# Kernel tuning notes

Hardware: AMD Instinct MI355X
Metric: run time of the kernel (lower is better)

## Reference

```python
import math
import jax, jax.numpy as jnp
import numpy as np

D_MODEL = 1024
NUM_SCALES = 4
STATE_SIZE = 16
EXPAND = 2
D_INNER = D_MODEL * EXPAND
D_PER_SCALE = D_INNER // NUM_SCALES
BATCH, SEQ = 4, 4096


def _make_A_log():
    base = np.arange(1, STATE_SIZE + 1, dtype=np.float32)  # (N,)
    parts = [np.broadcast_to(base * (2.0 ** i), (D_PER_SCALE, STATE_SIZE)) for i in range(NUM_SCALES)]
    A = np.concatenate(parts, axis=0)  # (d_inner, N)
    return jnp.asarray(np.log(A))


def setup_inputs() -> dict:
    key = jax.random.key(0)
    ks = jax.random.split(key, 8)
    scale = 0.02
    x = jax.random.normal(ks[0], (BATCH, SEQ, D_MODEL), dtype=jnp.float32)
    W_in = jax.random.normal(ks[1], (2 * D_INNER, D_MODEL), dtype=jnp.float32) * scale
    W_B = jax.random.normal(ks[2], (STATE_SIZE, D_INNER), dtype=jnp.float32) * scale
    W_C = jax.random.normal(ks[3], (STATE_SIZE, D_INNER), dtype=jnp.float32) * scale
    W_dt = jax.random.normal(ks[4], (D_INNER, D_INNER), dtype=jnp.float32) * scale
    # dt bias: log of dt_init ~ Uniform in log-space between 1e-3 and 1e-1
    u = jax.random.uniform(ks[5], (D_INNER,), dtype=jnp.float32)
    b_dt = u * (math.log(0.1) - math.log(0.001)) + math.log(0.001)
    W_out = jax.random.normal(ks[6], (D_MODEL, D_INNER), dtype=jnp.float32) * scale
    A_log = _make_A_log()
    D = jnp.ones((D_INNER,), dtype=jnp.float32)
    output_gate = jnp.zeros((1,), dtype=jnp.float32)
    return {"x": x, "W_in": W_in, "A_log": A_log, "W_B": W_B, "W_C": W_C,
            "W_dt": W_dt, "b_dt": b_dt, "D": D, "output_gate": output_gate, "W_out": W_out}


def _selective_scan(x_ssm, A, B_mat, C_mat, dt):
    # x_ssm: (B,L,d), A: (d,N), B_mat/C_mat: (B,L,N), dt: (B,L,d)
    b, L, d = x_ssm.shape
    N = A.shape[1]
    h0 = jnp.zeros((b, d, N), dtype=jnp.float32)

    def step(h, inp):
        dt_t, B_t, C_t, x_t = inp  # (B,d),(B,N),(B,N),(B,d)
        A_bar = jnp.exp(jnp.minimum(dt_t[..., None] * A, 20.0))       # (B,d,N)
        B_bar = dt_t[..., None] * B_t[:, None, :]                      # (B,d,N)
        h = A_bar * h + B_bar * x_t[..., None]
        y_t = jnp.einsum('bdn,bn->bd', h, C_t)
        return h, y_t

    xs = (jnp.swapaxes(dt, 0, 1), jnp.swapaxes(B_mat, 0, 1),
          jnp.swapaxes(C_mat, 0, 1), jnp.swapaxes(x_ssm, 0, 1))
    _, ys = jax.lax.scan(step, h0, xs)   # ys: (L,B,d)
    return jnp.swapaxes(ys, 0, 1)


def reference(x, W_in, A_log, W_B, W_C, W_dt, b_dt, D, output_gate, W_out):
    xz = jnp.einsum('bld,ed->ble', x, W_in)          # (B,L,2*d_inner)
    x_ssm, z = jnp.split(xz, 2, axis=-1)
    A = -jnp.exp(A_log.astype(jnp.float32))           # (d_inner,N)
    B_mat = jnp.einsum('bld,nd->bln', x_ssm, W_B)
    C_mat = jnp.einsum('bld,nd->bln', x_ssm, W_C)
    dt = jax.nn.softplus(jnp.einsum('bld,ed->ble', x_ssm, W_dt) + b_dt)
    y = _selective_scan(x_ssm.astype(jnp.float32), A,
                        B_mat.astype(jnp.float32), C_mat.astype(jnp.float32),
                        dt.astype(jnp.float32))
    y = y + x_ssm * D[None, None, :]
    y = y * jax.nn.silu(z)
    out = jnp.einsum('ble,de->bld', y, W_out) * jax.nn.sigmoid(output_gate)
    return out
```

## Files before the change

### kernel.cpp

```cpp
#include <hip/hip_runtime.h>
#include <hip/hip_bf16.h>
#include <math.h>

#define D_MODEL 1024
#define D_INNER 2048
#define NSTATE  16
#define BATCH   4
#define SEQ     4096
#define MTOT    (BATCH*SEQ)
#define SDT     2176
#define NCAT    2176
#define NCHUNK  16
#define CLEN    (SEQ/NCHUNK)
#define N1      (2*D_INNER)

typedef __attribute__((ext_vector_type(8))) __bf16 bf16x8;
typedef __attribute__((ext_vector_type(4))) float f32x4;

__device__ __forceinline__ float b2f(unsigned short u){
  return __uint_as_float(((unsigned int)u) << 16);
}
__device__ __forceinline__ unsigned short f2b(float f){
  unsigned int u = __float_as_uint(f);
  u = (u + 0x7FFFu + ((u >> 16) & 1u)) >> 16;
  return (unsigned short)u;
}
__device__ __forceinline__ float softplus_f(float x){
  float r = log1pf(__expf(-fabsf(x)));
  return x > 0.f ? x + r : r;
}

__device__ __forceinline__ void async16(unsigned short* lds, const unsigned short* g){
  __builtin_amdgcn_global_load_lds(
      (const __attribute__((address_space(1))) unsigned int*)g,
      (__attribute__((address_space(3))) unsigned int*)lds, 16, 0, 0);
}

__global__ void cvt_f2b_kernel(const float* __restrict__ src,
                               unsigned short* __restrict__ dst){
  int i = (blockIdx.x * 256 + threadIdx.x) * 4;
  float4 v = *(const float4*)(src + i);
  *(ushort2*)(dst + i)     = (ushort2){f2b(v.x), f2b(v.y)};
  *(ushort2*)(dst + i + 2) = (ushort2){f2b(v.z), f2b(v.w)};
}

__global__ void concat_w_kernel(const float* __restrict__ Wdt,
                                const float* __restrict__ WB,
                                const float* __restrict__ WC,
                                unsigned short* __restrict__ Wcat){
  int idx = blockIdx.x * 256 + threadIdx.x;
  int row = idx >> 9;
  int q   = idx & 511;
  float4 v;
  if      (row < 2048) v = *(const float4*)(Wdt + ((size_t)row * 2048 + q * 4));
  else if (row < 2064) v = *(const float4*)(WB  + ((size_t)(row - 2048) * 2048 + q * 4));
  else if (row < 2080) v = *(const float4*)(WC  + ((size_t)(row - 2064) * 2048 + q * 4));
  else                 v = make_float4(0.f, 0.f, 0.f, 0.f);
  unsigned short* p = Wcat + (size_t)idx * 4;
  *(ushort2*)(p)     = (ushort2){f2b(v.x), f2b(v.y)};
  *(ushort2*)(p + 2) = (ushort2){f2b(v.z), f2b(v.w)};
}

template<int MODE, int K>
__global__ __launch_bounds__(512, 1) void gemm_bt(
    const unsigned short* __restrict__ A,
    const unsigned short* __restrict__ W,
    unsigned short* __restrict__ o0,
    unsigned short* __restrict__ o1,
    float* __restrict__ of,
    const float* __restrict__ bias)
{
  const int tid  = threadIdx.x;
  const int lane = tid & 63;
  const int w    = tid >> 6;
  const int wm   = w >> 2;
  const int wn   = w & 3;
  const int m16  = lane & 15, q = lane >> 4;

  const int gx  = gridDim.x;
  const int nwg = gx * gridDim.y;
  int flat = blockIdx.y * gx + blockIdx.x;
  flat = (flat & 7) * (nwg >> 3) + (flat >> 3);
  const int bm = flat / gx;
  const int bn = flat - bm * gx;

  __shared__ unsigned short sA[2][16384];
  __shared__ unsigned short sB[2][8192];

  f32x4 acc[8][2];
  #pragma unroll
  for (int i = 0; i < 8; i++)
    #pragma unroll
    for (int j = 0; j < 2; j++) acc[i][j] = (f32x4){0.f, 0.f, 0.f, 0.f};

  const int ch = (tid & 7) ^ ((tid >> 3) & 7);
  const unsigned short* Ag = A + (size_t)(bm * 256 + (tid >> 3)) * K + ch * 8;
  const unsigned short* Wg = W + (size_t)(bn * 128 + (tid >> 3)) * K + ch * 8;

#define STAGE_A(buf, h, t) do { \
    async16(&sA[buf][(h)*8192 + w*512],        Ag + (size_t)((h)*128    )*K + (t)*64); \
    async16(&sA[buf][(h)*8192 + 4096 + w*512], Ag + (size_t)((h)*128 + 64)*K + (t)*64); \
  } while(0)
#define STAGE_B(buf, t) do { \
    async16(&sB[buf][w*512],        Wg + (size_t)(t)*64); \
    async16(&sB[buf][4096 + w*512], Wg + (size_t)64*K + (t)*64); \
  } while(0)

#define LDA(dst, buf, mh) do { \
    _Pragma("unroll") for (int mt = 0; mt < 4; mt++) \
    _Pragma("unroll") for (int kk = 0; kk < 2; kk++) { \
      const int row_ = wm*128 + (mh)*64 + mt*16 + m16; \
      dst[mt][kk] = *(const bf16x8*)&sA[buf][row_*64 + (((kk*4 + q) ^ (m16 & 7)) << 3)]; \
    } } while(0)
#define LDB(dst, buf) do { \
    _Pragma("unroll") for (int nt = 0; nt < 2; nt++) \
    _Pragma("unroll") for (int kk = 0; kk < 2; kk++) { \
      const int row_ = wn*32 + nt*16 + m16; \
      dst[nt][kk] = *(const bf16x8*)&sB[buf][row_*64 + (((kk*4 + q) ^ (m16 & 7)) << 3)]; \
    } } while(0)

#define MMAQ(Aa, Bb, MH) do { \
    __builtin_amdgcn_s_setprio(1); \
    _Pragma("unroll") for (int kk = 0; kk < 2; kk++) \
    _Pragma("unroll") for (int mt = 0; mt < 4; mt++) \
    _Pragma("unroll") for (int nt = 0; nt < 2; nt++) \
      acc[(MH)*4 + mt][nt] = __builtin_amdgcn_mfma_f32_16x16x32_bf16( \
          Aa[mt][kk], Bb[nt][kk], acc[(MH)*4 + mt][nt], 0, 0, 0); \
    __builtin_amdgcn_s_setprio(0); \
    __builtin_amdgcn_sched_barrier(0); \
  } while(0)

#define BAR()  asm volatile("s_barrier" ::: "memory")
#define LGK0() do { asm volatile("s_waitcnt lgkmcnt(0)" ::: "memory"); \
                    __builtin_amdgcn_sched_barrier(0); } while(0)

  STAGE_A(0, 0, 0); STAGE_A(0, 1, 0); STAGE_B(0, 0);
  STAGE_A(1, 0, 1); STAGE_A(1, 1, 1);
  asm volatile("s_waitcnt vmcnt(4)" ::: "memory");
  BAR();

  auto run_iter = [&](int t0, bool last) {
    bf16x8 a[4][2], b[2][2];
    LDA(a, 0, 0); LDB(b, 0);
    STAGE_B(1, t0 + 1);
    BAR(); LGK0();
    MMAQ(a, b, 0);
    BAR();
    LDA(a, 0, 1);
    if (!last) { STAGE_A(0, 0, t0 + 2); STAGE_A(0, 1, t0 + 2); }
    BAR(); LGK0();
    MMAQ(a, b, 1);
    if (last) asm volatile("s_waitcnt vmcnt(0)" ::: "memory");
    else      asm volatile("s_waitcnt vmcnt(4)" ::: "memory");
    BAR();
    LDA(a, 1, 0); LDB(b, 1);
    if (!last) STAGE_B(0, t0 + 2);
    BAR(); LGK0();
    MMAQ(a, b, 0);
    BAR();
    LDA(a, 1, 1);
    if (!last) { STAGE_A(1, 0, t0 + 3); STAGE_A(1, 1, t0 + 3); }
    BAR(); LGK0();
    MMAQ(a, b, 1);
    if (!last) asm volatile("s_waitcnt vmcnt(4)" ::: "memory");
    BAR();
  };

  const int NIT = K >> 7;
  #pragma unroll 1
  for (int j = 0; j < NIT - 1; j++) run_iter(2 * j, false);
  run_iter(2 * (NIT - 1), true);

  float gscale = 1.f;
  if (MODE == 2) gscale = 1.f / (1.f + __expf(-bias[0]));

  const int r0 = bm * 256 + wm * 128 + (q << 2);
  const int c0 = bn * 128 + wn * 32 + m16;
  #pragma unroll
  for (int mt = 0; mt < 8; mt++) {
    #pragma unroll
    for (int nt = 0; nt < 2; nt++) {
      const int col = c0 + nt * 16;
      #pragma unroll
      for (int i = 0; i < 4; i++) {
        const int row = r0 + mt * 16 + i;
        float v = acc[mt][nt][i];
        if (MODE == 0) {
          if (col < D_INNER) o0[(size_t)row * D_INNER + col] = f2b(v);
          else               o1[(size_t)row * D_INNER + (col - D_INNER)] = f2b(v);
        } else if (MODE == 1) {
          if (col < D_INNER) v = softplus_f(v + bias[col]);
          o0[(size_t)row * SDT + col] = f2b(v);
        } else {
          of[(size_t)row * D_MODEL + col] = v * gscale;
        }
      }
    }
  }
#undef STAGE_A
#undef STAGE_B
#undef LDA
#undef LDB
#undef MMAQ
#undef BAR
#undef LGK0
}

__global__ __launch_bounds__(256) void scan_passA(
    const unsigned short* __restrict__ dtBC,
    const unsigned short* __restrict__ xs,
    const float* __restrict__ Alog,
    float* __restrict__ Pb, float* __restrict__ Sb)
{
  const int d = blockIdx.x * 256 + threadIdx.x;
  const int b = blockIdx.y;
  const int c = blockIdx.z;

  float a[NSTATE];
  #pragma unroll
  for (int n = 0; n < NSTATE; n++) a[n] = -__expf(Alog[d * NSTATE + n]);

  float P[NSTATE], S[NSTATE];
  #pragma unroll
  for (int n = 0; n < NSTATE; n++) { P[n] = 1.f; S[n] = 0.f; }

  __shared__ float sB[16][16];
  const size_t bL = (size_t)b * SEQ;
  const int t0c = c * CLEN;
  const int lt = threadIdx.x >> 4, ln = threadIdx.x & 15;

  for (int t0 = t0c; t0 < t0c + CLEN; t0 += 16) {
    __syncthreads();
    sB[lt][ln] = b2f(dtBC[(bL + t0 + lt) * SDT + 2048 + ln]);
    __syncthreads();
    for (int tt = 0; tt < 16; tt++) {
      const size_t rw = bL + t0 + tt;
      const float dt = b2f(dtBC[rw * SDT + d]);
      const float x  = b2f(xs[rw * D_INNER + d]);
      const float dtx = dt * x;
      #pragma unroll
      for (int n = 0; n < NSTATE; n++) {
        const float ab = __expf(dt * a[n]);
        P[n] *= ab;
        S[n] = ab * S[n] + dtx * sB[tt][n];
      }
    }
  }
  const size_t base = (((size_t)c * BATCH + b) * D_INNER + d) * NSTATE;
  #pragma unroll
  for (int n = 0; n < NSTATE; n += 4) {
    *(f32x4*)&Pb[base + n] = (f32x4){P[n], P[n+1], P[n+2], P[n+3]};
    *(f32x4*)&Sb[base + n] = (f32x4){S[n], S[n+1], S[n+2], S[n+3]};
  }
}

__global__ __launch_bounds__(256) void scan_passB(float* __restrict__ Pb,
                                                  const float* __restrict__ Sb)
{
  const size_t j = (size_t)blockIdx.x * 256 + threadIdx.x;
  const size_t stride = (size_t)BATCH * D_INNER * NSTATE;
  float h = 0.f;
  for (int c = 0; c < NCHUNK; c++) {
    const size_t idx = (size_t)c * stride + j;
    const float p = Pb[idx];
    const float s = Sb[idx];
    Pb[idx] = h;
    h = p * h + s;
  }
}

__global__ __launch_bounds__(256) void scan_passC(
    const unsigned short* __restrict__ dtBC,
    const unsigned short* __restrict__ xs,
    const unsigned short* __restrict__ zb,
    const float* __restrict__ Alog,
    const float* __restrict__ Dv,
    const float* __restrict__ Hb,
    unsigned short* __restrict__ yb)
{
  const int d = blockIdx.x * 256 + threadIdx.x;
  const int b = blockIdx.y;
  const int c = blockIdx.z;

  float a[NSTATE];
  #pragma unroll
  for (int n = 0; n < NSTATE; n++) a[n] = -__expf(Alog[d * NSTATE + n]);

  float h[NSTATE];
  const size_t base = (((size_t)c * BATCH + b) * D_INNER + d) * NSTATE;
  #pragma unroll
  for (int n = 0; n < NSTATE; n += 4) {
    f32x4 v = *(const f32x4*)&Hb[base + n];
    h[n] = v.x; h[n+1] = v.y; h[n+2] = v.z; h[n+3] = v.w;
  }
  const float Dd = Dv[d];

  __shared__ float sB[16][16];
  __shared__ float sC[16][16];
  const size_t bL = (size_t)b * SEQ;
  const int t0c = c * CLEN;
  const int lt = threadIdx.x >> 4, ln = threadIdx.x & 15;

  for (int t0 = t0c; t0 < t0c + CLEN; t0 += 16) {
    __syncthreads();
    {
      const size_t rwb = (bL + t0 + lt) * SDT + 2048;
      sB[lt][ln] = b2f(dtBC[rwb + ln]);
      sC[lt][ln] = b2f(dtBC[rwb + 16 + ln]);
    }
    __syncthreads();
    for (int tt = 0; tt < 16; tt++) {
      const size_t rw = bL + t0 + tt;
      const float dt = b2f(dtBC[rw * SDT + d]);
      const float x  = b2f(xs[rw * D_INNER + d]);
      const float z  = b2f(zb[rw * D_INNER + d]);
      const float dtx = dt * x;
      float y = 0.f;
      #pragma unroll
      for (int n = 0; n < NSTATE; n++) {
        const float ab = __expf(dt * a[n]);
        h[n] = ab * h[n] + dtx * sB[tt][n];
        y += h[n] * sC[tt][n];
      }
      y = (y + x * Dd) * (z / (1.f + __expf(-z)));
      yb[rw * D_INNER + d] = f2b(y);
    }
  }
}

extern "C" void kernel_launch(void* const* d_in, const int* in_sizes, int n_in,
                              void* d_out, int out_size, void* d_ws, size_t ws_size,
                              hipStream_t stream)
{
  const float* x    = (const float*)d_in[0];
  const float* Win  = (const float*)d_in[1];
  const float* Alog = (const float*)d_in[2];
  const float* WB   = (const float*)d_in[3];
  const float* WC   = (const float*)d_in[4];
  const float* Wdt  = (const float*)d_in[5];
  const float* bdt  = (const float*)d_in[6];
  const float* Dv   = (const float*)d_in[7];
  const float* gate = (const float*)d_in[8];
  const float* Wout = (const float*)d_in[9];
  float* outp = (float*)d_out;

  char* ws = (char*)d_ws;
  unsigned short* xs    = (unsigned short*)(ws + 0);
  unsigned short* zy    = (unsigned short*)(ws + 67108864);
  unsigned short* dtBC  = (unsigned short*)(ws + 134217728);
  unsigned short* Winb  = (unsigned short*)(ws + 205520896);
  unsigned short* Woutb = (unsigned short*)(ws + 213909504);

  char* ob = (char*)d_out;
  float* Pb = (float*)(ob + 0);
  float* Sb = (float*)(ob + 8388608);
  unsigned short* Wcatb = (unsigned short*)(ob + 16777216);
  unsigned short* xb    = (unsigned short*)(ob + 33554432);

  cvt_f2b_kernel<<<16384, 256, 0, stream>>>(x, xb);
  cvt_f2b_kernel<<<4096, 256, 0, stream>>>(Win, Winb);
  cvt_f2b_kernel<<<2048, 256, 0, stream>>>(Wout, Woutb);
  concat_w_kernel<<<(NCAT * D_INNER / 4) / 256, 256, 0, stream>>>(Wdt, WB, WC, Wcatb);

  gemm_bt<0, D_MODEL><<<dim3(N1 / 128, MTOT / 256), 512, 0, stream>>>(
      xb, Winb, xs, zy, nullptr, nullptr);
  gemm_bt<1, D_INNER><<<dim3(NCAT / 128, MTOT / 256), 512, 0, stream>>>(
      xs, Wcatb, dtBC, nullptr, nullptr, bdt);
  scan_passA<<<dim3(D_INNER / 256, BATCH, NCHUNK), 256, 0, stream>>>(
      dtBC, xs, Alog, Pb, Sb);
  scan_passB<<<(BATCH * D_INNER * NSTATE) / 256, 256, 0, stream>>>(Pb, Sb);
  scan_passC<<<dim3(D_INNER / 256, BATCH, NCHUNK), 256, 0, stream>>>(
      dtBC, xs, zy, Alog, Dv, Pb, zy);
  gemm_bt<2, D_INNER><<<dim3(D_MODEL / 128, MTOT / 256), 512, 0, stream>>>(
      zy, Woutb, nullptr, nullptr, outp, gate);
}
```

Baseline: 1.108 ms.

## Reshape GEMM wave tiling to 4x2 waves of 64x64 and template grid width

```diff
diff --git a/kernel.cpp b/kernel.cpp
--- a/kernel.cpp
+++ b/kernel.cpp
@@ -61,7 +61,7 @@
   *(ushort2*)(p + 2) = (ushort2){f2b(v.z), f2b(v.w)};
 }
 
-template<int MODE, int K>
+template<int MODE, int K, int GX>
 __global__ __launch_bounds__(512, 1) void gemm_bt(
     const unsigned short* __restrict__ A,
     const unsigned short* __restrict__ W,
@@ -73,25 +73,24 @@
   const int tid  = threadIdx.x;
   const int lane = tid & 63;
   const int w    = tid >> 6;
-  const int wm   = w >> 2;
-  const int wn   = w & 3;
+  const int wm   = w >> 1;
+  const int wn   = w & 1;
   const int m16  = lane & 15, q = lane >> 4;
 
-  const int gx  = gridDim.x;
-  const int nwg = gx * gridDim.y;
-  int flat = blockIdx.y * gx + blockIdx.x;
-  flat = (flat & 7) * (nwg >> 3) + (flat >> 3);
-  const int bm = flat / gx;
-  const int bn = flat - bm * gx;
+  constexpr int NWG = GX * (MTOT / 256);
+  int flat = blockIdx.y * GX + blockIdx.x;
+  flat = (flat & 7) * (NWG >> 3) + (flat >> 3);
+  const int bm = flat / GX;
+  const int bn = flat - bm * GX;
 
   __shared__ unsigned short sA[2][16384];
   __shared__ unsigned short sB[2][8192];
 
-  f32x4 acc[8][2];
-  #pragma unroll
-  for (int i = 0; i < 8; i++)
+  f32x4 acc[4][4];
+  #pragma unroll
+  for (int i = 0; i < 4; i++)
     #pragma unroll
-    for (int j = 0; j < 2; j++) acc[i][j] = (f32x4){0.f, 0.f, 0.f, 0.f};
+    for (int j = 0; j < 4; j++) acc[i][j] = (f32x4){0.f, 0.f, 0.f, 0.f};
 
   const int ch = (tid & 7) ^ ((tid >> 3) & 7);
   const unsigned short* Ag = A + (size_t)(bm * 256 + (tid >> 3)) * K + ch * 8;
@@ -106,33 +105,31 @@
     async16(&sB[buf][4096 + w*512], Wg + (size_t)64*K + (t)*64); \
   } while(0)
 
-#define LDA(dst, buf, mh) do { \
+#define LDA(dst, buf) do { \
     _Pragma("unroll") for (int mt = 0; mt < 4; mt++) \
     _Pragma("unroll") for (int kk = 0; kk < 2; kk++) { \
-      const int row_ = wm*128 + (mh)*64 + mt*16 + m16; \
+      const int row_ = wm*64 + mt*16 + m16; \
       dst[mt][kk] = *(const bf16x8*)&sA[buf][row_*64 + (((kk*4 + q) ^ (m16 & 7)) << 3)]; \
     } } while(0)
-#define LDB(dst, buf) do { \
+#define LDB(dst, buf, nh) do { \
     _Pragma("unroll") for (int nt = 0; nt < 2; nt++) \
     _Pragma("unroll") for (int kk = 0; kk < 2; kk++) { \
-      const int row_ = wn*32 + nt*16 + m16; \
+      const int row_ = wn*64 + (nh)*32 + nt*16 + m16; \
       dst[nt][kk] = *(const bf16x8*)&sB[buf][row_*64 + (((kk*4 + q) ^ (m16 & 7)) << 3)]; \
     } } while(0)
 
-#define MMAQ(Aa, Bb, MH) do { \
+#define MMAQ(Aa, Bb, NH) do { \
     __builtin_amdgcn_s_setprio(1); \
     _Pragma("unroll") for (int kk = 0; kk < 2; kk++) \
     _Pragma("unroll") for (int mt = 0; mt < 4; mt++) \
     _Pragma("unroll") for (int nt = 0; nt < 2; nt++) \
-      acc[(MH)*4 + mt][nt] = __builtin_amdgcn_mfma_f32_16x16x32_bf16( \
-          Aa[mt][kk], Bb[nt][kk], acc[(MH)*4 + mt][nt], 0, 0, 0); \
+      acc[mt][(NH)*2 + nt] = __builtin_amdgcn_mfma_f32_16x16x32_bf16( \
+          Aa[mt][kk], Bb[nt][kk], acc[mt][(NH)*2 + nt], 0, 0, 0); \
     __builtin_amdgcn_s_setprio(0); \
-    __builtin_amdgcn_sched_barrier(0); \
   } while(0)
 
 #define BAR()  asm volatile("s_barrier" ::: "memory")
-#define LGK0() do { asm volatile("s_waitcnt lgkmcnt(0)" ::: "memory"); \
-                    __builtin_amdgcn_sched_barrier(0); } while(0)
+#define LGK0() asm volatile("s_waitcnt lgkmcnt(0)" ::: "memory")
 
   STAGE_A(0, 0, 0); STAGE_A(0, 1, 0); STAGE_B(0, 0);
   STAGE_A(1, 0, 1); STAGE_A(1, 1, 1);
@@ -141,24 +138,24 @@
 
   auto run_iter = [&](int t0, bool last) {
     bf16x8 a[4][2], b[2][2];
-    LDA(a, 0, 0); LDB(b, 0);
+    LDA(a, 0); LDB(b, 0, 0);
     STAGE_B(1, t0 + 1);
     BAR(); LGK0();
     MMAQ(a, b, 0);
     BAR();
-    LDA(a, 0, 1);
+    LDB(b, 0, 1);
     if (!last) { STAGE_A(0, 0, t0 + 2); STAGE_A(0, 1, t0 + 2); }
     BAR(); LGK0();
     MMAQ(a, b, 1);
     if (last) asm volatile("s_waitcnt vmcnt(0)" ::: "memory");
     else      asm volatile("s_waitcnt vmcnt(4)" ::: "memory");
     BAR();
-    LDA(a, 1, 0); LDB(b, 1);
+    LDA(a, 1); LDB(b, 1, 0);
     if (!last) STAGE_B(0, t0 + 2);
     BAR(); LGK0();
     MMAQ(a, b, 0);
     BAR();
-    LDA(a, 1, 1);
+    LDB(b, 1, 1);
     if (!last) { STAGE_A(1, 0, t0 + 3); STAGE_A(1, 1, t0 + 3); }
     BAR(); LGK0();
     MMAQ(a, b, 1);
@@ -166,7 +163,7 @@
     BAR();
   };
 
-  const int NIT = K >> 7;
+  constexpr int NIT = K >> 7;
   #pragma unroll 1
   for (int j = 0; j < NIT - 1; j++) run_iter(2 * j, false);
   run_iter(2 * (NIT - 1), true);
@@ -174,12 +171,12 @@
   float gscale = 1.f;
   if (MODE == 2) gscale = 1.f / (1.f + __expf(-bias[0]));
 
-  const int r0 = bm * 256 + wm * 128 + (q << 2);
-  const int c0 = bn * 128 + wn * 32 + m16;
-  #pragma unroll
-  for (int mt = 0; mt < 8; mt++) {
+  const int r0 = bm * 256 + wm * 64 + (q << 2);
+  const int c0 = bn * 128 + wn * 64 + m16;
+  #pragma unroll
+  for (int mt = 0; mt < 4; mt++) {
     #pragma unroll
-    for (int nt = 0; nt < 2; nt++) {
+    for (int nt = 0; nt < 4; nt++) {
       const int col = c0 + nt * 16;
       #pragma unroll
       for (int i = 0; i < 4; i++) {
@@ -362,15 +359,15 @@
   cvt_f2b_kernel<<<2048, 256, 0, stream>>>(Wout, Woutb);
   concat_w_kernel<<<(NCAT * D_INNER / 4) / 256, 256, 0, stream>>>(Wdt, WB, WC, Wcatb);
 
-  gemm_bt<0, D_MODEL><<<dim3(N1 / 128, MTOT / 256), 512, 0, stream>>>(
+  gemm_bt<0, D_MODEL, N1 / 128><<<dim3(N1 / 128, MTOT / 256), 512, 0, stream>>>(
       xb, Winb, xs, zy, nullptr, nullptr);
-  gemm_bt<1, D_INNER><<<dim3(NCAT / 128, MTOT / 256), 512, 0, stream>>>(
+  gemm_bt<1, D_INNER, NCAT / 128><<<dim3(NCAT / 128, MTOT / 256), 512, 0, stream>>>(
       xs, Wcatb, dtBC, nullptr, nullptr, bdt);
   scan_passA<<<dim3(D_INNER / 256, BATCH, NCHUNK), 256, 0, stream>>>(
       dtBC, xs, Alog, Pb, Sb);
   scan_passB<<<(BATCH * D_INNER * NSTATE) / 256, 256, 0, stream>>>(Pb, Sb);
   scan_passC<<<dim3(D_INNER / 256, BATCH, NCHUNK), 256, 0, stream>>>(
       dtBC, xs, zy, Alog, Dv, Pb, zy);
-  gemm_bt<2, D_INNER><<<dim3(D_MODEL / 128, MTOT / 256), 512, 0, stream>>>(
+  gemm_bt<2, D_INNER, D_MODEL / 128><<<dim3(D_MODEL / 128, MTOT / 256), 512, 0, stream>>>(
       zy, Woutb, nullptr, nullptr, outp, gate);
 }
```

Result: no change. 1.101 ms (-0.6%).
